# Optimization experiments

Measured on AMD Instinct MI355X. Metric: run time of the kernel, lower is better.

The kernel has to match this reference:

```python
import jax, jax.numpy as jnp
import numpy as np

L = 16          # quantization levels (MSB LUT)
UP = 2          # upscale factor
H, W = 2048, 2048

# neighbor offsets (x, y) for pixels b and c per kernel type: 'h', 'd', 'b'
_OFFSETS = [((0, 1), (0, 2)),   # h: horizontal
            ((1, 1), (2, 2)),   # d: diagonal
            ((1, 2), (2, 1))]   # b: anti-diagonal-ish


def setup_inputs() -> dict:
    key = jax.random.key(0)
    k1, k2 = jax.random.split(key)
    img_lr = jax.random.randint(k1, (H, W), 0, L, dtype=jnp.int32)
    msb_weight = jax.random.normal(k2, (3, L ** 3, UP * UP), dtype=jnp.float32)
    return {"img_lr": img_lr, "msb_weight": msb_weight}


def reference(img_lr, msb_weight):
    up = UP
    out = jnp.zeros((img_lr.shape[0] * up, img_lr.shape[1] * up), jnp.float32)
    for k in range(3):  # kernel types h, d, b
        (xb, yb), (xc, yc) = _OFFSETS[k]
        w = msb_weight[k]                         # [L^3, up*up]
        for r in range(4):                        # 4-fold rotation ensemble
            rot = jnp.rot90(img_lr, r)            # get_slice rotation
            dx, dy = rot.shape
            p = jnp.pad(rot, ((0, 2), (0, 2)), mode='reflect')
            a = p[:dx, :dy]                       # anchor pixel (0,0)
            b = p[xb:xb + dx, yb:yb + dy]
            c = p[xc:xc + dx, yc:yc + dy]
            idx = (a * (L * L) + b * L + c).reshape(-1)  # composite LUT index
            # gather, then interleave the up x up sub-pixels spatially
            tmp = w[idx].reshape(dx, dy, up, up)
            tmp = tmp.transpose(0, 2, 1, 3).reshape(dx * up, dy * up)
            out = out + jnp.rot90(tmp, (4 - r) % 4)      # rotate back
    return out / 3.0
```

## Files before the change

### kernel.cpp

```cpp
#include <hip/hip_runtime.h>
#include <hip/hip_fp16.h>

#define N 2048
#define ONW 4096
#define TW 128
#define TH 32
#define HW 132
#define HH 36
#define HELEMS (HW * HH)
#define LUT_ENTRIES 12288
#define LUT_BYTES (LUT_ENTRIES * 8)
#define SMEM_BYTES (LUT_BYTES + 2 * HELEMS * 4)

typedef _Float16 half4v __attribute__((ext_vector_type(4)));
typedef float fvec4 __attribute__((ext_vector_type(4)));

__device__ __forceinline__ int reflect(int i) {
    i = i < 0 ? -i : i;
    return i >= N ? 2 * N - 2 - i : i;
}

__global__ __launch_bounds__(1024, 4) void hdblut_kernel(
    const int* __restrict__ img, const float4* __restrict__ w4,
    float* __restrict__ out)
{
    extern __shared__ unsigned char smem[];
    half4v* lut = (half4v*)smem;
    int* bufs = (int*)(smem + LUT_BYTES);

    const int tx = threadIdx.x;
    const int ty = threadIdx.y;
    const int tid = ty * 64 + tx;
    const int x0 = (int)(blockIdx.x & 15) * TW;
    const int y0 = (int)(blockIdx.x >> 4) * (TH * 4);

    #pragma unroll
    for (int i = 0; i < 12; ++i) {
        int j = tid + i * 1024;
        float4 v = w4[j];
        half4v h;
        h.x = (_Float16)v.x; h.y = (_Float16)v.y;
        h.z = (_Float16)v.z; h.w = (_Float16)v.w;
        lut[j] = h;
    }

    for (int e = tid; e < HELEMS; e += 1024) {
        int rr = e / HW, cc = e - rr * HW;
        bufs[e] = img[reflect(y0 + rr - 2) * N + reflect(x0 + cc - 2)];
    }
    __syncthreads();

    const int bo[3][2] = {{0, 1}, {1, 1}, {1, 2}};
    const int co[3][2] = {{0, 2}, {2, 2}, {2, 1}};
    const float s = 1.0f / 3.0f;
    fvec4* o4 = (fvec4*)out;

    int pre[5];
    #pragma unroll 1
    for (int t = 0; t < 4; ++t) {
        int* cur = bufs + (t & 1) * HELEMS;
        int* nxt = bufs + ((t + 1) & 1) * HELEMS;

        if (t < 3) {
            const int yb = y0 + (t + 1) * TH;
            #pragma unroll
            for (int u = 0; u < 5; ++u) {
                int e = tid + u * 1024;
                if (e < HELEMS) {
                    int rr = e / HW, cc = e - rr * HW;
                    pre[u] = img[reflect(yb + rr - 2) * N + reflect(x0 + cc - 2)];
                }
            }
        }

        int n[6][6];
        {
            const int r0 = 2 * ty, c0 = 2 * tx;
            #pragma unroll
            for (int r = 0; r < 6; ++r)
                #pragma unroll
                for (int j = 0; j < 3; ++j) {
                    int2 t2 = *(const int2*)&cur[(r0 + r) * HW + c0 + 2 * j];
                    n[r][2 * j] = t2.x; n[r][2 * j + 1] = t2.y;
                }
        }

        float acc[2][2][4];
        #pragma unroll
        for (int i = 0; i < 2; ++i)
            #pragma unroll
            for (int j = 0; j < 2; ++j)
                #pragma unroll
                for (int c = 0; c < 4; ++c) acc[i][j][c] = 0.f;

        #pragma unroll
        for (int pi = 0; pi < 2; ++pi) {
            int idx[24];
            #pragma unroll
            for (int pj = 0; pj < 2; ++pj) {
                const int a8 = n[2 + pi][2 + pj] << 8;
                #pragma unroll
                for (int r = 0; r < 4; ++r) {
                    #pragma unroll
                    for (int k = 0; k < 3; ++k) {
                        const int bp = bo[k][0], bq = bo[k][1];
                        const int cp = co[k][0], cq = co[k][1];
                        const int bdi = (r == 0) ? bp : (r == 1) ? bq : (r == 2) ? -bp : -bq;
                        const int bdj = (r == 0) ? bq : (r == 1) ? -bp : (r == 2) ? -bq : bp;
                        const int cdi = (r == 0) ? cp : (r == 1) ? cq : (r == 2) ? -cp : -cq;
                        const int cdj = (r == 0) ? cq : (r == 1) ? -cp : (r == 2) ? -cq : cp;
                        const int bv = n[pi + 2 + bdi][pj + 2 + bdj];
                        const int cv = n[pi + 2 + cdi][pj + 2 + cdj];
                        idx[pj * 12 + r * 3 + k] = (k * 4096 + a8) + (bv * 16 + cv);
                    }
                }
            }
            half4v v[24];
            #pragma unroll
            for (int i = 0; i < 24; ++i) v[i] = lut[idx[i]];
            __builtin_amdgcn_sched_group_barrier(0x100, 24, 0);

            #pragma unroll
            for (int pj = 0; pj < 2; ++pj) {
                float* o = acc[pi][pj];
                #pragma unroll
                for (int r = 0; r < 4; ++r) {
                    half4v S = v[pj * 12 + 3 * r] + v[pj * 12 + 3 * r + 1]
                                                  + v[pj * 12 + 3 * r + 2];
                    const float x = (float)S.x, y = (float)S.y;
                    const float z = (float)S.z, w = (float)S.w;
                    if (r == 0)      { o[0] += x; o[1] += y; o[2] += z; o[3] += w; }
                    else if (r == 1) { o[0] += z; o[1] += x; o[2] += w; o[3] += y; }
                    else if (r == 2) { o[0] += w; o[1] += z; o[2] += y; o[3] += x; }
                    else             { o[0] += y; o[1] += w; o[2] += x; o[3] += z; }
                }
            }
        }

        const int py = y0 + t * TH + 2 * ty;
        const int ox = (x0 + 2 * tx) * 2;
        {
            fvec4 v0 = {acc[0][0][0] * s, acc[0][0][1] * s, acc[0][1][0] * s, acc[0][1][1] * s};
            fvec4 v1 = {acc[0][0][2] * s, acc[0][0][3] * s, acc[0][1][2] * s, acc[0][1][3] * s};
            fvec4 v2 = {acc[1][0][0] * s, acc[1][0][1] * s, acc[1][1][0] * s, acc[1][1][1] * s};
            fvec4 v3 = {acc[1][0][2] * s, acc[1][0][3] * s, acc[1][1][2] * s, acc[1][1][3] * s};
            o4[((2 * py + 0) * ONW + ox) >> 2] = v0;
            o4[((2 * py + 1) * ONW + ox) >> 2] = v1;
            o4[((2 * py + 2) * ONW + ox) >> 2] = v2;
            o4[((2 * py + 3) * ONW + ox) >> 2] = v3;
        }

        if (t < 3) {
            #pragma unroll
            for (int u = 0; u < 5; ++u) {
                int e = tid + u * 1024;
                if (e < HELEMS) nxt[e] = pre[u];
            }
        }
        __syncthreads();
    }
}

extern "C" void kernel_launch(void* const* d_in, const int* in_sizes, int n_in,
                              void* d_out, int out_size, void* d_ws, size_t ws_size,
                              hipStream_t stream)
{
    const int* img = (const int*)d_in[0];
    const float4* w4 = (const float4*)d_in[1];
    float* out = (float*)d_out;
    (void)hipFuncSetAttribute(reinterpret_cast<const void*>(hdblut_kernel),
                              hipFuncAttributeMaxDynamicSharedMemorySize, SMEM_BYTES);
    hdblut_kernel<<<dim3(256), dim3(64, 16), SMEM_BYTES, stream>>>(img, w4, out);
}
```

Before: 94.38 us.

## Stage image tiles via async global-to-LDS loads and batch both LUT gather rows

Replaces the register-staged prefetch of the next image halo tile with direct global_load_lds transfers into the alternate LDS buffer, which removes the register round trip and the explicit LDS stores. The LUT gathers for both pixel rows are also issued back-to-back before accumulation, so more LDS loads are in flight at once. Correctness depends on global_load_lds writing each wave's elements contiguously at lds_buf+ebase and on those loads completing before the __syncthreads. The second change raises register pressure (48 half4 values live at once) under a 1024-thread launch bound, which risks spilling.

```diff
diff --git a/kernel.cpp b/kernel.cpp
--- a/kernel.cpp
+++ b/kernel.cpp
@@ -20,6 +20,24 @@
     return i >= N ? 2 * N - 2 - i : i;
 }
 
+__device__ __forceinline__ void stage_tile_async(
+    const int* __restrict__ img, int* lds_buf, int x0, int yb, int ty, int tx)
+{
+    #pragma unroll
+    for (int u = 0; u < 5; ++u) {
+        const int ebase = ty * 64 + u * 1024;
+        const int e = ebase + tx;
+        if (e < HELEMS) {
+            const int rr = e / HW, cc = e - rr * HW;
+            const int* src = img + reflect(yb + rr - 2) * N + reflect(x0 + cc - 2);
+            __builtin_amdgcn_global_load_lds(
+                (const __attribute__((address_space(1))) void*)src,
+                (__attribute__((address_space(3))) void*)(lds_buf + ebase),
+                4, 0, 0);
+        }
+    }
+}
+
 __global__ __launch_bounds__(1024, 4) void hdblut_kernel(
     const int* __restrict__ img, const float4* __restrict__ w4,
     float* __restrict__ out)
@@ -34,6 +52,8 @@
     const int x0 = (int)(blockIdx.x & 15) * TW;
     const int y0 = (int)(blockIdx.x >> 4) * (TH * 4);
 
+    stage_tile_async(img, bufs, x0, y0, ty, tx);
+
     #pragma unroll
     for (int i = 0; i < 12; ++i) {
         int j = tid + i * 1024;
@@ -43,11 +63,6 @@
         h.z = (_Float16)v.z; h.w = (_Float16)v.w;
         lut[j] = h;
     }
-
-    for (int e = tid; e < HELEMS; e += 1024) {
-        int rr = e / HW, cc = e - rr * HW;
-        bufs[e] = img[reflect(y0 + rr - 2) * N + reflect(x0 + cc - 2)];
-    }
     __syncthreads();
 
     const int bo[3][2] = {{0, 1}, {1, 1}, {1, 2}};
@@ -55,23 +70,13 @@
     const float s = 1.0f / 3.0f;
     fvec4* o4 = (fvec4*)out;
 
-    int pre[5];
     #pragma unroll 1
     for (int t = 0; t < 4; ++t) {
         int* cur = bufs + (t & 1) * HELEMS;
         int* nxt = bufs + ((t + 1) & 1) * HELEMS;
 
-        if (t < 3) {
-            const int yb = y0 + (t + 1) * TH;
-            #pragma unroll
-            for (int u = 0; u < 5; ++u) {
-                int e = tid + u * 1024;
-                if (e < HELEMS) {
-                    int rr = e / HW, cc = e - rr * HW;
-                    pre[u] = img[reflect(yb + rr - 2) * N + reflect(x0 + cc - 2)];
-                }
-            }
-        }
+        if (t < 3)
+            stage_tile_async(img, nxt, x0, y0 + (t + 1) * TH, ty, tx);
 
         int n[6][6];
         {
@@ -93,9 +98,9 @@
                 #pragma unroll
                 for (int c = 0; c < 4; ++c) acc[i][j][c] = 0.f;
 
+        int idx[2][24];
         #pragma unroll
         for (int pi = 0; pi < 2; ++pi) {
-            int idx[24];
             #pragma unroll
             for (int pj = 0; pj < 2; ++pj) {
                 const int a8 = n[2 + pi][2 + pj] << 8;
@@ -111,15 +116,23 @@
                         const int cdj = (r == 0) ? cq : (r == 1) ? -cp : (r == 2) ? -cq : cp;
                         const int bv = n[pi + 2 + bdi][pj + 2 + bdj];
                         const int cv = n[pi + 2 + cdi][pj + 2 + cdj];
-                        idx[pj * 12 + r * 3 + k] = (k * 4096 + a8) + (bv * 16 + cv);
+                        idx[pi][pj * 12 + r * 3 + k] = (k * 4096 + a8) + (bv * 16 + cv);
                     }
                 }
             }
-            half4v v[24];
-            #pragma unroll
-            for (int i = 0; i < 24; ++i) v[i] = lut[idx[i]];
-            __builtin_amdgcn_sched_group_barrier(0x100, 24, 0);
+        }
 
+        half4v vA[24], vB[24];
+        #pragma unroll
+        for (int i = 0; i < 24; ++i) vA[i] = lut[idx[0][i]];
+        __builtin_amdgcn_sched_group_barrier(0x100, 24, 0);
+        #pragma unroll
+        for (int i = 0; i < 24; ++i) vB[i] = lut[idx[1][i]];
+        __builtin_amdgcn_sched_group_barrier(0x100, 24, 0);
+
+        #pragma unroll
+        for (int pi = 0; pi < 2; ++pi) {
+            half4v* v = (pi == 0) ? vA : vB;
             #pragma unroll
             for (int pj = 0; pj < 2; ++pj) {
                 float* o = acc[pi][pj];
@@ -150,13 +163,6 @@
             o4[((2 * py + 3) * ONW + ox) >> 2] = v3;
         }
 
-        if (t < 3) {
-            #pragma unroll
-            for (int u = 0; u < 5; ++u) {
-                int e = tid + u * 1024;
-                if (e < HELEMS) nxt[e] = pre[u];
-            }
-        }
         __syncthreads();
     }
 }
```

Result: no change. 94.92 us (+0.6%).
